# Performance work log

Hardware: AMD Instinct MI355X
Metric: run time of the kernel (lower is better)

The kernel has to match this reference:

```python
import jax, jax.numpy as jnp
import numpy as np

B, P, K = 8, 1024, 20
N = B * P
EMB, OUT = 1024, 40
GRID = 5

def _window(W):
    # Hamming taper (window_type='hamming')
    n = jnp.arange(W, dtype=jnp.float32)
    return 0.54 - 0.46 * jnp.cos(2.0 * jnp.pi * n / (W - 1))

def _init_kan(key, din, dout, W, S, g):
    nw = (din - W) // S + 1
    coeffs = jax.random.normal(key, (2, dout, nw, W, g), jnp.float32) / (np.sqrt(nw * W) * np.sqrt(g))
    bias = jnp.zeros((dout,), jnp.float32)
    return coeffs, bias

def stft_kan(x, coeffs, bias, W, S):
    # x: (n, D) -> (n, dout). Slice D into overlapping windows of size W,
    # stride S, apply Hamming taper, build Fourier features cos(k*x), sin(k*x)
    # for k=1..g and contract with learned coefficients (STFT-Fourier-KAN).
    nw, g = coeffs.shape[2], coeffs.shape[4]
    idx = (np.arange(nw) * S)[:, None] + np.arange(W)[None, :]        # (nw, W)
    xw = x[:, idx] * _window(W)                                        # (n, nw, W)
    kfreq = jnp.arange(1, g + 1, dtype=x.dtype)
    arg = xw[..., None] * kfreq                                        # (n, nw, W, g)
    y = (jnp.einsum('nwig,owig->no', jnp.cos(arg), coeffs[0])
         + jnp.einsum('nwig,owig->no', jnp.sin(arg), coeffs[1]))
    return y + bias

def setup_inputs():
    key = jax.random.key(0)
    ks = jax.random.split(key, 5)
    pos = jax.random.normal(ks[0], (N, 3), jnp.float32)
    batch = (jnp.arange(N) // P).astype(jnp.int32)  # sorted, equal-size clouds
    c1, b1 = _init_kan(ks[1], 6, 64, 3, 3, GRID)
    c2, b2 = _init_kan(ks[2], 64, 128, 16, 8, GRID)
    c3, b3 = _init_kan(ks[3], 128, EMB, 32, 16, GRID)
    c4, b4 = _init_kan(ks[4], 2 * EMB, OUT, 256, 128, GRID)
    return {"pos": pos, "batch": batch, "c1": c1, "b1": b1, "c2": c2, "b2": b2,
            "c3": c3, "b3": b3, "c4": c4, "b4": b4}

def reference(pos, batch, c1, b1, c2, b2, c3, b3, c4, b4):
    posb = pos.reshape(B, P, 3)
    # dynamic kNN graph per cloud (self excluded)
    d = jnp.sum((posb[:, :, None, :] - posb[:, None, :, :]) ** 2, -1)  # (B,P,P)
    d = d + jnp.eye(P, dtype=d.dtype) * 1e10
    _, nbr = jax.lax.top_k(-d, K)                                      # (B,P,K)
    pj = jax.vmap(lambda p, i: p[i])(posb, nbr)                        # (B,P,K,3)
    pi = jnp.broadcast_to(posb[:, :, None, :], pj.shape)
    e = jnp.concatenate([pi, pj - pi], -1).reshape(N * K, 6)           # edge feats
    h = stft_kan(e, c1, b1, 3, 3)                                      # (N*K,64)
    h = stft_kan(h, c2, b2, 16, 8)                                     # (N*K,128)
    x1 = jnp.max(h.reshape(N, K, 128), axis=1)                         # max aggr over neighbors
    x = stft_kan(x1, c3, b3, 32, 16)                                   # (N,EMB)
    gmax = jax.ops.segment_max(x, batch, num_segments=B)
    gsum = jax.ops.segment_sum(x, batch, num_segments=B)
    cnt = jax.ops.segment_sum(jnp.ones((N, 1), x.dtype), batch, num_segments=B)
    xg = jnp.concatenate([gmax, gsum / cnt], -1)                       # (B, 2*EMB)
    return stft_kan(xg, c4, b4, 256, 128)                              # (B, OUT)
```

## Files before the change

kernel.cpp:

```cpp
#include <hip/hip_runtime.h>


typedef unsigned short u16;
typedef unsigned int   u32;
typedef unsigned long long u64;
typedef __attribute__((ext_vector_type(8))) _Float16 half8;
typedef __attribute__((ext_vector_type(4))) float f32x4;

__device__ __forceinline__ float bf2f(u16 u) {
  u32 v = ((u32)u) << 16;
  return __uint_as_float(v);
}
__device__ __forceinline__ u16 f2bfr(float f) {
  u32 x = __float_as_uint(f);
  u32 r = x + 0x7FFFu + ((x >> 16) & 1u);
  return (u16)(r >> 16);
}
__device__ __forceinline__ u16 f2h(float f) {
  _Float16 h = (_Float16)f;
  u16 r;
  __builtin_memcpy(&r, &h, 2);
  return r;
}
__device__ __forceinline__ float h2f(u16 u) {
  _Float16 h;
  __builtin_memcpy(&h, &u, 2);
  return (float)h;
}
__device__ __forceinline__ float ldf(const void* p, size_t i, bool f32) {
  return f32 ? ((const float*)p)[i] : bf2f(((const u16*)p)[i]);
}
__device__ __forceinline__ u64 minu64(u64 a, u64 b) { return a < b ? a : b; }

#define NBR_OFF   ((size_t)0)
#define FLAG_OFF  ((size_t)917504)
#define XG_OFF    ((size_t)(1u << 20))
#define L4P_OFF   (((size_t)(1u << 20)) + 131072)
#define C1T_OFF   (((size_t)(1u << 20)) + 524288)
#define C2T_OFF   (((size_t)(1u << 20)) + 589824)
#define C3T_OFF   ((size_t)(2u << 20))
#define C4T_OFF   ((size_t)(7u << 20))
#define PMAX_OFF  ((size_t)(13u << 20))
#define PSUM_OFF  ((size_t)(14u << 20))
#define X1_OFF    ((size_t)(15u << 20))
#define H1_OFF    ((size_t)(18u << 20))

__global__ void detect_kernel(const void* __restrict__ pos,
                              int* __restrict__ flag) {
  int t = threadIdx.x;
  float a = fabsf(((const float*)pos)[t]);
  bool ok = (a > 1.0e-3f && a < 100.0f);
  unsigned long long m = __ballot(ok);
  if (t == 0) *flag = (__popcll(m) >= 32) ? 1 : 0;
}

__global__ void tkan_kernel(const void* __restrict__ src, void* __restrict__ dst,
                            int dout, int nw, int W, int total, int KPAD,
                            int outf32, const int* __restrict__ dfl) {
  int id = blockIdx.x * 256 + threadIdx.x;
  if (id >= total) return;
  const bool f32 = (*dfl != 0);
  int o = id / KPAD, f = id % KPAD;
  int NA = nw * W;
  int Kt = NA * 10;
  float v = 0.f;
  if (f < Kt) {
    int part = f & 1, p = f >> 1;
    int aa, gg;
    if (p < 4 * NA) { aa = p >> 2;      gg = p & 3; }
    else            { aa = p - 4 * NA;  gg = 4;     }
    int i = aa % W, w = aa / W;
    int OS = NA * 5;
    size_t sidx = (size_t)part * (dout * OS) + (size_t)o * OS + w * (W * 5) + i * 5 + gg;
    v = ldf(src, sidx, f32);
  }
  if (outf32) ((float*)dst)[id] = v;
  else        ((u16*)dst)[id] = f2h(v);
}

__global__ __launch_bounds__(256) void knn_kernel(const void* __restrict__ pos,
                                                  int* __restrict__ nbr,
                                                  const int* __restrict__ dfl) {
  __shared__ float px[1024], py[1024], pz[1024];
  const bool f32 = (*dfl != 0);
  const int t = threadIdx.x;
  const int b = blockIdx.y;
  const int base = b << 10;
  for (int j = t; j < 1024; j += 256) {
    size_t pidx = (size_t)(base + j) * 3;
    px[j] = ldf(pos, pidx, f32);
    py[j] = ldf(pos, pidx + 1, f32);
    pz[j] = ldf(pos, pidx + 2, f32);
  }
  __syncthreads();
  const int wv = t >> 6, lane = t & 63;
  const int q = blockIdx.x * 4 + wv;
  const float qx = px[q], qy = py[q], qz = pz[q];
  u64 key[16];
#pragma unroll
  for (int s = 0; s < 16; ++s) {
    const int j = s * 64 + lane;
    float dx = qx - px[j], dy = qy - py[j], dz = qz - pz[j];
    float d = __fadd_rn(__fadd_rn(__fmul_rn(dx, dx), __fmul_rn(dy, dy)),
                        __fmul_rn(dz, dz));
    key[s] = (j == q) ? ~0ull
                      : ((((u64)__float_as_uint(d)) << 32) | (u32)j);
  }
  const int obase = (base + q) * 20;
  for (int k = 0; k < 20; ++k) {
    u64 m = key[0];
#pragma unroll
    for (int s = 1; s < 16; ++s) m = minu64(m, key[s]);
#pragma unroll
    for (int off = 32; off >= 1; off >>= 1) {
      u32 lo = (u32)m, hi = (u32)(m >> 32);
      lo = __shfl_xor(lo, off, 64);
      hi = __shfl_xor(hi, off, 64);
      m = minu64(m, (((u64)hi) << 32) | lo);
    }
    if (lane == 0) nbr[obase + k] = (int)(u32)m;
#pragma unroll
    for (int s = 0; s < 16; ++s)
      if (key[s] == m) key[s] = ~0ull;
  }
}

template <int L>
__global__ __launch_bounds__(256, (L == 2) ? 2 : 3) void kan_kernel(
    const void* __restrict__ in_, const int* __restrict__ nbr,
    const void* __restrict__ pos, const u16* __restrict__ ct,
    const void* __restrict__ bias, void* __restrict__ out_,
    float* __restrict__ pmax, float* __restrict__ psum,
    const int* __restrict__ dfl) {
  constexpr int W    = (L == 1) ? 3  : (L == 2) ? 16  : 32;
  constexpr int S    = (L == 1) ? 3  : (L == 2) ? 8   : 16;
  constexpr int DIN  = (L == 1) ? 6  : (L == 2) ? 64  : 128;
  constexpr int NT   = 64;
  constexpr int NW   = (DIN - W) / S + 1;
  constexpr int NA   = NW * W;
  constexpr int NPAIR = NA * 5;
  constexpr int S1P  = NA * 4;
  constexpr int KROW  = (L == 1) ? 64 : NPAIR * 2;
  constexpr int NCH   = KROW / 32;
  constexpr int NB    = NT / 16;
  constexpr int RW    = (L == 1) ? 64 : (L == 2) ? 80 : 32;
  constexpr int MB    = RW / 16;
  constexpr int PSTH  = DIN + 8;
  constexpr int LGW   = (W == 16) ? 4 : 5;
  constexpr int BBS   = 4 * 520;

  __shared__ float hamS[(L == 1) ? 1 : W];
  __shared__ float wT1[(L == 1) ? 32 : 1];
  __shared__ int   hT1[(L == 1) ? 32 : 1];
  __shared__ u16   slab[(L == 1) ? 2 : 4 * RW * PSTH];
  __shared__ u16   stage1[(L == 1) ? 4 * 64 * 64 : 2];
  __shared__ u16   Bbuf[2 * BBS];

  const bool f32 = (*dfl != 0);
  const u16* inH = (const u16*)in_;
  const int t = threadIdx.x;
  if constexpr (L == 1) {
    if (t < 32) {
      float wv_ = 0.f; int hx = 0;
      if (t < NPAIR) {
        int aa, gg;
        if (t < S1P) { aa = t >> 2;   gg = t & 3; }
        else         { aa = t - S1P;  gg = 4;     }
        int i = aa % W;
        float hm = 0.54f - 0.46f * cospif(2.0f * (float)i / (float)(W - 1));
        wv_ = hm * (float)(gg + 1);
        hx = aa;
      }
      wT1[t] = wv_; hT1[t] = hx;
    }
  } else {
    if (t < W) hamS[t] = 0.54f - 0.46f * cospif(2.0f * (float)t / (float)(W - 1));
  }

  int tile, ncol0;
  if constexpr (L == 3) {
    const int id = blockIdx.x;
    tile = (id >> 3) & 63;
    ncol0 = ((((id & 7) << 1) | (id >> 9))) * NT;
  } else {
    tile = blockIdx.x;
    ncol0 = blockIdx.y * NT;
  }
  const int lane = t & 63, wv = t >> 6;
  const int m16 = lane & 15, kb = lane >> 4;
  const int rowbase = tile * (4 * RW) + wv * RW;
  u16* myslab = &slab[(L == 1) ? 0 : wv * RW * PSTH];

  const int scol = t >> 2, spart = t & 3;
  const u16* srcB = ct + (size_t)(ncol0 + scol) * KROW + spart * 8;

  if constexpr (L >= 2) {
    constexpr int F16R = DIN / 8;
    constexpr int TOT = RW * F16R;
    for (int i = lane; i < TOT; i += 64) {
      const int r = i / F16R, c8 = i % F16R;
      *(uint4*)(myslab + r * PSTH + c8 * 8) =
          *(const uint4*)(inH + (size_t)(rowbase + r) * DIN + c8 * 8);
    }
  }

  {
    const uint4 v = *(const uint4*)srcB;
    *(uint4*)(Bbuf + spart * 520 + scol * 8) = v;
  }
  __syncthreads();

  f32x4 acc[MB][NB];
#pragma unroll
  for (int mb = 0; mb < MB; ++mb)
#pragma unroll
    for (int nb = 0; nb < NB; ++nb) {
      acc[mb][nb][0] = 0.f; acc[mb][nb][1] = 0.f;
      acc[mb][nb][2] = 0.f; acc[mb][nb][3] = 0.f;
    }

  for (int c = 0; c < NCH; ++c) {
    uint4 bnext;
    const bool havenext = (c + 1 < NCH);
    if (havenext)
      bnext = *(const uint4*)(srcB + (c + 1) * 32);
    const int pg0 = c * 16 + kb * 4;
    half8 af[MB];
    if constexpr (L == 1) {
      float wm[4]; int hx[4]; bool val[4];
#pragma unroll
      for (int u = 0; u < 4; ++u) {
        const int pg = pg0 + u;
        wm[u] = wT1[pg]; hx[u] = hT1[pg]; val[u] = (pg < NPAIR);
      }
#pragma unroll
      for (int mb = 0; mb < MB; ++mb) {
        const int row = rowbase + mb * 16 + m16;
        const int pt = row / 20;
        const int cloud = pt >> 10, ci = pt & 1023;
        const int cb = cloud << 10;
        const int jl = nbr[row];
#pragma unroll
        for (int u = 0; u < 4; ++u) {
          float cs = 0.f, sn = 0.f;
          if (val[u]) {
            const int aa = hx[u];
            float v;
            if (aa < 3) {
              v = ldf(pos, (size_t)(cb + ci) * 3 + aa, f32);
            } else {
              const int cc2 = aa - 3;
              v = ldf(pos, (size_t)(cb + jl) * 3 + cc2, f32) -
                  ldf(pos, (size_t)(cb + ci) * 3 + cc2, f32);
            }
            const float ang = v * wm[u];
            cs = __cosf(ang); sn = __sinf(ang);
          }
          af[mb][2 * u]     = (_Float16)cs;
          af[mb][2 * u + 1] = (_Float16)sn;
        }
      }
    } else if (pg0 < S1P) {
      const int aa = pg0 >> 2;
      const int i = aa & (W - 1), w = aa >> LGW;
      const int hidx = S * w + i;
      const float hm = hamS[i];
#pragma unroll
      for (int mb = 0; mb < MB; ++mb) {
        const u16* rp = myslab + (mb * 16 + m16) * PSTH;
        const float th = h2f(rp[hidx]) * hm;
        const float c1 = __cosf(th), s1 = __sinf(th);
        const float tc = 2.0f * c1;
        const float c2 = tc * c1 - 1.0f, s2 = tc * s1;
        const float c3 = tc * c2 - c1,   s3 = tc * s2 - s1;
        const float c4 = tc * c3 - c2,   s4 = tc * s3 - s2;
        af[mb][0] = (_Float16)c1; af[mb][1] = (_Float16)s1;
        af[mb][2] = (_Float16)c2; af[mb][3] = (_Float16)s2;
        af[mb][4] = (_Float16)c3; af[mb][5] = (_Float16)s3;
        af[mb][6] = (_Float16)c4; af[mb][7] = (_Float16)s4;
      }
    } else {
      const int q0 = pg0 - S1P;
      float wm[4]; int hx[4];
#pragma unroll
      for (int u = 0; u < 4; ++u) {
        const int aa = q0 + u;
        const int i = aa & (W - 1), w = aa >> LGW;
        hx[u] = S * w + i;
        wm[u] = hamS[i] * 5.0f;
      }
#pragma unroll
      for (int mb = 0; mb < MB; ++mb) {
        const u16* rp = myslab + (mb * 16 + m16) * PSTH;
#pragma unroll
        for (int u = 0; u < 4; ++u) {
          const float ang = h2f(rp[hx[u]]) * wm[u];
          af[mb][2 * u]     = (_Float16)__cosf(ang);
          af[mb][2 * u + 1] = (_Float16)__sinf(ang);
        }
      }
    }
    const u16* bb = Bbuf + (c & 1) * BBS + kb * 520;
#pragma unroll
    for (int nb = 0; nb < NB; ++nb) {
      const half8 bv = *(const half8*)(bb + (nb * 16 + m16) * 8);
#pragma unroll
      for (int mb = 0; mb < MB; ++mb)
        acc[mb][nb] = __builtin_amdgcn_mfma_f32_16x16x32_f16(
            af[mb], bv, acc[mb][nb], 0, 0, 0);
    }
    if (havenext) {
      *(uint4*)(Bbuf + ((c + 1) & 1) * BBS + spart * 520 + scol * 8) = bnext;
      __syncthreads();
    }
  }

  if constexpr (L == 1) {
    u16* st = &stage1[wv * 4096];
#pragma unroll
    for (int mb = 0; mb < MB; ++mb)
#pragma unroll
      for (int nb = 0; nb < NB; ++nb) {
        const float bsv = ldf(bias, nb * 16 + m16, f32);
#pragma unroll
        for (int r = 0; r < 4; ++r)
          st[(mb * 16 + kb * 4 + r) * 64 + nb * 16 + m16] =
              f2h(acc[mb][nb][r] + bsv);
      }
    u16* gp = (u16*)out_ + (size_t)rowbase * 64;
    for (int i = lane; i < 512; i += 64)
      *(uint4*)(gp + i * 8) = *(const uint4*)&st[i * 8];
  } else if constexpr (L == 2) {
    u16* st = myslab;
#pragma unroll
    for (int mb = 0; mb < MB; ++mb)
#pragma unroll
      for (int nb = 0; nb < NB; ++nb) {
        const float bsv = ldf(bias, ncol0 + nb * 16 + m16, f32);
#pragma unroll
        for (int r = 0; r < 4; ++r)
          st[(mb * 16 + kb * 4 + r) * PSTH + nb * 16 + m16] =
              f2h(acc[mb][nb][r] + bsv);
      }
    const int pbase = tile * 16 + wv * 4;
#pragma unroll
    for (int j = 0; j < 4; ++j) {
      float m = -3.0e38f;
#pragma unroll
      for (int k = 0; k < 20; ++k)
        m = fmaxf(m, h2f(st[(j * 20 + k) * PSTH + lane]));
      ((u16*)out_)[(size_t)(pbase + j) * 128 + ncol0 + lane] = f2h(m);
    }
  } else {
    const int chunk = rowbase >> 5;
#pragma unroll
    for (int nb = 0; nb < NB; ++nb) {
      const int col = ncol0 + nb * 16 + m16;
      const float bsv = ldf(bias, col, f32);
      float m = -3.0e38f, s = 0.f;
#pragma unroll
      for (int mb = 0; mb < MB; ++mb)
#pragma unroll
        for (int r = 0; r < 4; ++r) {
          const float v = acc[mb][nb][r] + bsv;
          m = fmaxf(m, v); s += v;
        }
#pragma unroll
      for (int off = 16; off <= 32; off <<= 1) {
        m = fmaxf(m, __shfl_xor(m, off, 64));
        s += __shfl_xor(s, off, 64);
      }
      if (kb == 0) {
        pmax[(size_t)chunk * 1024 + col] = m;
        psum[(size_t)chunk * 1024 + col] = s;
      }
    }
  }
}

__global__ void seg2_kernel(const float* __restrict__ pmax,
                            const float* __restrict__ psum,
                            float* __restrict__ xg) {
  const int id = blockIdx.x * 256 + threadIdx.x;
  const int b = id >> 10, col = id & 1023;
  float m = -3.0e38f, s = 0.f;
  for (int rc = 0; rc < 32; ++rc) {
    m = fmaxf(m, pmax[(size_t)(b * 32 + rc) * 1024 + col]);
    s += psum[(size_t)(b * 32 + rc) * 1024 + col];
  }
  xg[b * 2048 + col] = m;
  xg[b * 2048 + 1024 + col] = s * (1.0f / 1024.0f);
}

__global__ __launch_bounds__(256) void l4_kernel(const float* __restrict__ xg,
                                                 const float* __restrict__ c4t,
                                                 float* __restrict__ part) {
  __shared__ float F[2560];
  const int t = threadIdx.x;
  const int w = blockIdx.x, b = blockIdx.y;
  const float xv = xg[b * 2048 + w * 128 + t];
  const float hm = 0.54f - 0.46f * cospif(2.0f * (float)t / 255.0f);
  const float aa = xv * hm;
  const float c1 = __cosf(aa), s1 = __sinf(aa);
  const float tc = 2.0f * c1;
  const float c2 = tc * c1 - 1.0f, s2 = tc * s1;
  const float c3 = tc * c2 - c1,   s3 = tc * s2 - s1;
  const float c4 = tc * c3 - c2,   s4 = tc * s3 - s2;
  const float a5 = aa * 5.0f;
  F[t * 8]     = c1; F[t * 8 + 1] = s1;
  F[t * 8 + 2] = c2; F[t * 8 + 3] = s2;
  F[t * 8 + 4] = c3; F[t * 8 + 5] = s3;
  F[t * 8 + 6] = c4; F[t * 8 + 7] = s4;
  F[2048 + t * 2]     = __cosf(a5);
  F[2048 + t * 2 + 1] = __sinf(a5);
  __syncthreads();
  if (t < 240) {
    const int o = t % 40, s = t / 40;
    const int f0 = s * 432;
    const int f1 = (f0 + 432 < 2560) ? (f0 + 432) : 2560;
    const float* cp1 = c4t + (size_t)o * 38400 + w * 2048;
    const float* cp2 = c4t + (size_t)o * 38400 + 30720 + w * 512;
    float acc = 0.f;
    for (int f = f0; f < f1; f += 4) {
      const float* cpf = (f < 2048) ? (cp1 + f) : (cp2 + (f - 2048));
      const float4 cv = *(const float4*)cpf;
      const float4 fa = *(const float4*)&F[f];
      acc += fa.x * cv.x + fa.y * cv.y + fa.z * cv.z + fa.w * cv.w;
    }
    part[((b * 15 + w) * 6 + s) * 40 + o] = acc;
  }
}

__global__ void outred_kernel(const float* __restrict__ part,
                              const void* __restrict__ b4,
                              void* __restrict__ outp,
                              const int* __restrict__ dfl) {
  int t = threadIdx.x;
  if (t >= 320) return;
  const bool f32 = (*dfl != 0);
  int b = t / 40, o = t % 40;
  float s = ldf(b4, o, f32);
  for (int w = 0; w < 15; ++w)
#pragma unroll
    for (int sl = 0; sl < 6; ++sl)
      s += part[((b * 15 + w) * 6 + sl) * 40 + o];
  if (f32) ((float*)outp)[t] = s;
  else     ((u16*)outp)[t] = f2bfr(s);
}

extern "C" void kernel_launch(void* const* d_in, const int* in_sizes, int n_in,
                              void* d_out, int out_size, void* d_ws,
                              size_t ws_size, hipStream_t stream) {
  (void)in_sizes; (void)n_in; (void)out_size; (void)ws_size;
  const void* pos = d_in[0];
  const void* c1 = d_in[2];
  const void* b1 = d_in[3];
  const void* c2 = d_in[4];
  const void* b2 = d_in[5];
  const void* c3 = d_in[6];
  const void* b3 = d_in[7];
  const void* c4 = d_in[8];
  const void* b4 = d_in[9];

  char* ws = (char*)d_ws;
  int* nbr   = (int*)(ws + NBR_OFF);
  int* flag  = (int*)(ws + FLAG_OFF);
  float* xg  = (float*)(ws + XG_OFF);
  float* l4p = (float*)(ws + L4P_OFF);
  u16* c1t   = (u16*)(ws + C1T_OFF);
  u16* c2t   = (u16*)(ws + C2T_OFF);
  u16* c3t   = (u16*)(ws + C3T_OFF);
  float* c4t = (float*)(ws + C4T_OFF);
  float* pmax = (float*)(ws + PMAX_OFF);
  float* psum = (float*)(ws + PSUM_OFF);
  u16* x1    = (u16*)(ws + X1_OFF);
  u16* h1    = (u16*)(ws + H1_OFF);

  detect_kernel<<<1, 64, 0, stream>>>(pos, flag);

  tkan_kernel<<<16, 256, 0, stream>>>(c1, c1t, 64, 2, 3, 64 * 64, 64, 0, flag);
  tkan_kernel<<<560, 256, 0, stream>>>(c2, c2t, 128, 7, 16, 128 * 1120, 1120, 0, flag);
  tkan_kernel<<<8960, 256, 0, stream>>>(c3, c3t, 1024, 7, 32, 1024 * 2240, 2240, 0, flag);
  tkan_kernel<<<6000, 256, 0, stream>>>(c4, c4t, 40, 15, 256, 40 * 38400, 38400, 1, flag);

  knn_kernel<<<dim3(256, 8), 256, 0, stream>>>(pos, nbr, flag);

  kan_kernel<1><<<640, 256, 0, stream>>>(nullptr, nbr, pos, c1t, b1, h1,
                                         nullptr, nullptr, flag);
  kan_kernel<2><<<dim3(512, 2), 256, 0, stream>>>(h1, nullptr, nullptr, c2t,
                                                  b2, x1, nullptr, nullptr, flag);
  kan_kernel<3><<<1024, 256, 0, stream>>>(x1, nullptr, nullptr, c3t,
                                          b3, nullptr, pmax, psum, flag);

  seg2_kernel<<<32, 256, 0, stream>>>(pmax, psum, xg);
  l4_kernel<<<dim3(15, 8), 256, 0, stream>>>(xg, c4t, l4p);
  outred_kernel<<<1, 320, 0, stream>>>(l4p, b4, d_out, flag);
}
```

Before: 314.6 us.

## Merge coefficient transpose launches and shrink slab padding for KAN kernels

Folds the four coefficient-transposition kernels into one launch that dispatches on block index, removing three launch gaps. It also changes the layer-2 launch bound from 2 to 3 waves per SIMD and reduces the shared slab row pad from 8 to 4 halves, which needs the slab fill to use 8-byte copies instead of 16-byte copies. The smaller pad and tighter register budget may change LDS bank conflicts and cause spills in layer 2. The narrower global and LDS copies also issue twice as many transactions.

```diff
diff --git a/kernel.cpp b/kernel.cpp
--- a/kernel.cpp
+++ b/kernel.cpp
@@ -54,10 +54,23 @@
   if (t == 0) *flag = (__popcll(m) >= 32) ? 1 : 0;
 }
 
-__global__ void tkan_kernel(const void* __restrict__ src, void* __restrict__ dst,
-                            int dout, int nw, int W, int total, int KPAD,
-                            int outf32, const int* __restrict__ dfl) {
-  int id = blockIdx.x * 256 + threadIdx.x;
+__global__ void tkan_all_kernel(const void* __restrict__ s1, void* __restrict__ d1,
+                                const void* __restrict__ s2, void* __restrict__ d2,
+                                const void* __restrict__ s3, void* __restrict__ d3,
+                                const void* __restrict__ s4, void* __restrict__ d4,
+                                const int* __restrict__ dfl) {
+  const int blk = blockIdx.x;
+  const void* src; void* dst;
+  int dout, nw, W, total, KPAD, outf32, base;
+  if (blk < 16)        { src = s1; dst = d1; dout = 64;   nw = 2;  W = 3;
+                         total = 64 * 64;     KPAD = 64;    outf32 = 0; base = 0; }
+  else if (blk < 576)  { src = s2; dst = d2; dout = 128;  nw = 7;  W = 16;
+                         total = 128 * 1120;  KPAD = 1120;  outf32 = 0; base = 16; }
+  else if (blk < 9536) { src = s3; dst = d3; dout = 1024; nw = 7;  W = 32;
+                         total = 1024 * 2240; KPAD = 2240;  outf32 = 0; base = 576; }
+  else                 { src = s4; dst = d4; dout = 40;   nw = 15; W = 256;
+                         total = 40 * 38400;  KPAD = 38400; outf32 = 1; base = 9536; }
+  int id = (blk - base) * 256 + threadIdx.x;
   if (id >= total) return;
   const bool f32 = (*dfl != 0);
   int o = id / KPAD, f = id % KPAD;
@@ -126,7 +139,7 @@
 }
 
 template <int L>
-__global__ __launch_bounds__(256, (L == 2) ? 2 : 3) void kan_kernel(
+__global__ __launch_bounds__(256, 3) void kan_kernel(
     const void* __restrict__ in_, const int* __restrict__ nbr,
     const void* __restrict__ pos, const u16* __restrict__ ct,
     const void* __restrict__ bias, void* __restrict__ out_,
@@ -145,7 +158,7 @@
   constexpr int NB    = NT / 16;
   constexpr int RW    = (L == 1) ? 64 : (L == 2) ? 80 : 32;
   constexpr int MB    = RW / 16;
-  constexpr int PSTH  = DIN + 8;
+  constexpr int PSTH  = DIN + 4;
   constexpr int LGW   = (W == 16) ? 4 : 5;
   constexpr int BBS   = 4 * 520;
 
@@ -195,12 +208,12 @@
   const u16* srcB = ct + (size_t)(ncol0 + scol) * KROW + spart * 8;
 
   if constexpr (L >= 2) {
-    constexpr int F16R = DIN / 8;
-    constexpr int TOT = RW * F16R;
+    constexpr int F4R = DIN / 4;
+    constexpr int TOT = RW * F4R;
     for (int i = lane; i < TOT; i += 64) {
-      const int r = i / F16R, c8 = i % F16R;
-      *(uint4*)(myslab + r * PSTH + c8 * 8) =
-          *(const uint4*)(inH + (size_t)(rowbase + r) * DIN + c8 * 8);
+      const int r = i / F4R, c4 = i % F4R;
+      *(uint2*)(myslab + r * PSTH + c4 * 4) =
+          *(const uint2*)(inH + (size_t)(rowbase + r) * DIN + c4 * 4);
     }
   }
 
@@ -478,10 +491,8 @@
 
   detect_kernel<<<1, 64, 0, stream>>>(pos, flag);
 
-  tkan_kernel<<<16, 256, 0, stream>>>(c1, c1t, 64, 2, 3, 64 * 64, 64, 0, flag);
-  tkan_kernel<<<560, 256, 0, stream>>>(c2, c2t, 128, 7, 16, 128 * 1120, 1120, 0, flag);
-  tkan_kernel<<<8960, 256, 0, stream>>>(c3, c3t, 1024, 7, 32, 1024 * 2240, 2240, 0, flag);
-  tkan_kernel<<<6000, 256, 0, stream>>>(c4, c4t, 40, 15, 256, 40 * 38400, 38400, 1, flag);
+  tkan_all_kernel<<<15536, 256, 0, stream>>>(c1, c1t, c2, c2t, c3, c3t,
+                                             c4, c4t, flag);
 
   knn_kernel<<<dim3(256, 8), 256, 0, stream>>>(pos, nbr, flag);
 
```

Measured after the change: 311.5 us. No clear change (-1.0%).
